# Performance work log

Hardware: AMD Instinct MI355X
Metric: run time of the kernel (lower is better)

## Reference

```python
import jax, jax.numpy as jnp
import numpy as np

NUM_POINTS = 7
SCALES = (0.25, 0.125, 0.0625, 0.03125)
LENS_AREA = (8, 25)
OUTPUT_SIZES = ((8, 32), (8, 64))
CANON_SCALE = 224.0  # LevelMapper defaults (ctor's 160 is not forwarded)
CANON_LVL = 4.0
K_MIN, K_MAX = 2.0, 5.0
EPS = 1e-6


def _boundary_interp(pts, wp):
    # pts: [N, n, 2] polyline; sample wp points uniformly in arc parameter
    n = pts.shape[1]
    u = (jnp.arange(wp, dtype=pts.dtype) + 0.5) / wp * (n - 1)
    i0 = jnp.clip(jnp.floor(u).astype(jnp.int32), 0, n - 2)
    f = (u - i0.astype(pts.dtype))[None, :, None]
    return pts[:, i0] * (1 - f) + pts[:, i0 + 1] * f  # [N, wp, 2]


def _make_grid(polys_norm, hp, wp):
    # polys_norm: [N, 2n, 2] normalized to [0,1]; first n = top l->r, last n = bottom l->r
    n = polys_norm.shape[1] // 2
    top = _boundary_interp(polys_norm[:, :n], wp)
    bot = _boundary_interp(polys_norm[:, n:], wp)
    v = ((jnp.arange(hp, dtype=polys_norm.dtype) + 0.5) / hp)[None, :, None, None]
    return top[:, None] * (1 - v) + bot[:, None] * v  # [N, hp, wp, 2] (x,y)


def _bilinear(feat, img_ids, grid):
    # feat [B,C,H,W]; grid normalized [0,1] image coords -> pixel coords of this level
    B, C, H, W = feat.shape
    x = grid[..., 0] * W - 0.5
    y = grid[..., 1] * H - 0.5
    x0 = jnp.floor(x)
    y0 = jnp.floor(y)
    wx = (x - x0)[..., None]
    wy = (y - y0)[..., None]
    x0i = x0.astype(jnp.int32)
    y0i = y0.astype(jnp.int32)
    ids = img_ids[:, None, None]

    def g(xi, yi):
        xc = jnp.clip(xi, 0, W - 1)
        yc = jnp.clip(yi, 0, H - 1)
        val = feat[ids, :, yc, xc]  # [N, hp, wp, C]
        m = ((xi >= 0) & (xi < W) & (yi >= 0) & (yi < H))[..., None]
        return val * m.astype(feat.dtype)

    out = (g(x0i, y0i) * (1 - wx) * (1 - wy)
           + g(x0i + 1, y0i) * wx * (1 - wy)
           + g(x0i, y0i + 1) * (1 - wx) * wy
           + g(x0i + 1, y0i + 1) * wx * wy)
    return jnp.transpose(out, (0, 3, 1, 2))  # [N, C, hp, wp]


def _forward(feats, polys, img_ids, lens):
    n = NUM_POINTS
    idx = list(range(n)) + list(range(n, 2 * n))[::-1]  # top l->r, bottom flipped l->r
    H0, W0 = feats[0].shape[-2:]
    wh = jnp.array([W0 / SCALES[0], H0 / SCALES[0]], dtype=feats[0].dtype)
    polys_norm = polys[:, idx] / wh
    # FPN level routing from bbox area of the polygon (boxlist.area heuristic)
    s = jnp.sqrt((polys[..., 0].max(1) - polys[..., 0].min(1))
                 * (polys[..., 1].max(1) - polys[..., 1].min(1)))
    lvl = jnp.clip(jnp.floor(CANON_LVL + jnp.log2(s / CANON_SCALE + EPS)),
                   K_MIN, K_MAX).astype(jnp.int32) - int(K_MIN)
    # text-length bucket -> pooler id (first bucket whose len_max >= len)
    thr = jnp.array(LENS_AREA[:-1], dtype=lens.dtype)
    pooler_id = jnp.sum(lens[:, None] > thr[None, :], axis=1).astype(jnp.int32)

    outs = []
    N, C = polys.shape[0], feats[0].shape[1]
    for pid, (hp, wp) in enumerate(OUTPUT_SIZES):
        grid = _make_grid(polys_norm, hp, wp)
        acc = jnp.zeros((N, C, hp, wp), feats[0].dtype)
        for l, f in enumerate(feats):
            sel = ((lvl == l) & (pooler_id == pid))[:, None, None, None]
            acc = jnp.where(sel, _bilinear(f, img_ids, grid), acc)
        outs.append(acc)
    return tuple(outs)


def setup_inputs() -> dict:
    B, C, H0, W0 = 2, 256, 200, 336
    N, n = 256, NUM_POINTS
    key = jax.random.key(0)
    k0, k1, k2, k3 = jax.random.split(key, 4)
    feat0 = jax.random.normal(k0, (B, C, H0, W0), jnp.float32)
    feat1 = jax.random.normal(k1, (B, C, H0 // 2, W0 // 2), jnp.float32)
    feat2 = jax.random.normal(k2, (B, C, H0 // 4, W0 // 4), jnp.float32)
    feat3 = jax.random.normal(k3, (B, C, H0 // 8, W0 // 8), jnp.float32)
    rng = np.random.default_rng(0)
    img_w, img_h = W0 / SCALES[0], H0 / SCALES[0]
    cx = rng.uniform(0.25, 0.75, N) * img_w
    cy = rng.uniform(0.2, 0.8, N) * img_h
    w = rng.uniform(40.0, 600.0, N)
    h = rng.uniform(16.0, 80.0, N)
    t = np.linspace(0.0, 1.0, n)
    top_x = cx[:, None] + (t[None, :] - 0.5) * w[:, None]
    top_y = cy[:, None] - h[:, None] / 2 + rng.uniform(-2, 2, (N, n))
    bot_y = cy[:, None] + h[:, None] / 2 + rng.uniform(-2, 2, (N, n))
    # stored polygon order: top l->r then bottom r->l (matches self.idx reorder)
    top = np.stack([top_x, top_y], -1)
    bot = np.stack([top_x[:, ::-1], bot_y[:, ::-1]], -1)
    polys = jnp.asarray(np.concatenate([top, bot], 1), jnp.float32)  # [N, 14, 2]
    img_ids = jnp.asarray(rng.integers(0, B, N), jnp.int32)
    lens = jnp.asarray(rng.integers(1, 25, N), jnp.int32)
    return {"feat0": feat0, "feat1": feat1, "feat2": feat2, "feat3": feat3,
            "polys": polys, "img_ids": img_ids, "lens": lens}


def reference(feat0, feat1, feat2, feat3, polys, img_ids, lens):
    return _forward((feat0, feat1, feat2, feat3), polys, img_ids, lens)
```

## Files before the change

kernel.cpp:

```cpp
#include <hip/hip_runtime.h>


#define NBOX 256
#define NCH  256
#define HP   8
#define CCHUNK 32
#define OUT0_ELEMS ((size_t)NBOX * NCH * HP * 32)

__global__ __launch_bounds__(256) void poly_pool_kernel(
    const float* __restrict__ f0, const float* __restrict__ f1,
    const float* __restrict__ f2, const float* __restrict__ f3,
    const float* __restrict__ polys, const int* __restrict__ img_ids,
    const int* __restrict__ lens, float* __restrict__ out)
{
    const int b    = blockIdx.y;
    const int pidk = blockIdx.z;
    const int wp   = pidk ? 64 : 32;
    const int npos = HP * wp;
    const int c0   = blockIdx.x * CCHUNK;
    const int tid  = threadIdx.x;

    float* outb = out + (pidk ? OUT0_ELEMS : 0) + (size_t)b * NCH * npos;

    const int pooler = (lens[b] > 8) ? 1 : 0;
    if (pooler != pidk) {
        float* p = outb + (size_t)c0 * npos;
        const int total = CCHUNK * npos;
        for (int k = tid; k < total; k += 256) p[k] = 0.0f;
        return;
    }

    __shared__ float pts[28];
    __shared__ int   soff[512][4];
    __shared__ float swt [512][4];

    if (tid < 28) pts[tid] = polys[b * 28 + tid];
    __syncthreads();

    float minx = pts[0], maxx = pts[0], miny = pts[1], maxy = pts[1];
#pragma unroll
    for (int k = 1; k < 14; ++k) {
        float x = pts[2 * k], y = pts[2 * k + 1];
        minx = fminf(minx, x); maxx = fmaxf(maxx, x);
        miny = fminf(miny, y); maxy = fmaxf(maxy, y);
    }
    float s = sqrtf((maxx - minx) * (maxy - miny));
    int lvl = (int)floorf(4.0f + log2f(s / 224.0f + 1e-6f));
    lvl = min(max(lvl, 2), 5) - 2;

    const float* feat; int H, W;
    switch (lvl) {
        case 0:  feat = f0; H = 200; W = 336; break;
        case 1:  feat = f1; H = 100; W = 168; break;
        case 2:  feat = f2; H = 50;  W = 84;  break;
        default: feat = f3; H = 25;  W = 42;  break;
    }
    const int img = img_ids[b];
    const float* featimg = feat + (size_t)img * NCH * H * W;

    const float Wf = (float)W, Hf = (float)H;
    for (int pos = tid; pos < npos; pos += 256) {
        int i = pos / wp, j = pos % wp;

        float u = ((j + 0.5f) / (float)wp) * 6.0f;
        int   i0 = (int)floorf(u);
        i0 = min(max(i0, 0), 5);
        float f = u - (float)i0;

        float txa = pts[2 * i0]       / 1344.0f, tya = pts[2 * i0 + 1] / 800.0f;
        float txb = pts[2 * i0 + 2]   / 1344.0f, tyb = pts[2 * i0 + 3] / 800.0f;
        int ka = 13 - i0, kb = 12 - i0;
        float bxa = pts[2 * ka] / 1344.0f, bya = pts[2 * ka + 1] / 800.0f;
        float bxb = pts[2 * kb] / 1344.0f, byb = pts[2 * kb + 1] / 800.0f;

        float topx = txa * (1.0f - f) + txb * f;
        float topy = tya * (1.0f - f) + tyb * f;
        float botx = bxa * (1.0f - f) + bxb * f;
        float boty = bya * (1.0f - f) + byb * f;

        float v  = (i + 0.5f) / 8.0f;
        float gx = topx * (1.0f - v) + botx * v;
        float gy = topy * (1.0f - v) + boty * v;

        float x = gx * Wf - 0.5f;
        float y = gy * Hf - 0.5f;
        float x0f = floorf(x), y0f = floorf(y);
        float fx = x - x0f,   fy = y - y0f;
        int x0 = (int)x0f, y0 = (int)y0f;
        int x1 = x0 + 1,   y1 = y0 + 1;

        int x0c = min(max(x0, 0), W - 1), x1c = min(max(x1, 0), W - 1);
        int y0c = min(max(y0, 0), H - 1), y1c = min(max(y1, 0), H - 1);
        float m00 = (x0 >= 0 && x0 < W && y0 >= 0 && y0 < H) ? 1.0f : 0.0f;
        float m10 = (x1 >= 0 && x1 < W && y0 >= 0 && y0 < H) ? 1.0f : 0.0f;
        float m01 = (x0 >= 0 && x0 < W && y1 >= 0 && y1 < H) ? 1.0f : 0.0f;
        float m11 = (x1 >= 0 && x1 < W && y1 >= 0 && y1 < H) ? 1.0f : 0.0f;

        soff[pos][0] = y0c * W + x0c;
        soff[pos][1] = y0c * W + x1c;
        soff[pos][2] = y1c * W + x0c;
        soff[pos][3] = y1c * W + x1c;
        swt [pos][0] = (1.0f - fx) * (1.0f - fy) * m00;
        swt [pos][1] = fx * (1.0f - fy) * m10;
        swt [pos][2] = (1.0f - fx) * fy * m01;
        swt [pos][3] = fx * fy * m11;
    }
    __syncthreads();

    const int p0 = tid;
    int   o00 = soff[p0][0], o10 = soff[p0][1], o01 = soff[p0][2], o11 = soff[p0][3];
    float w00 = swt[p0][0],  w10 = swt[p0][1],  w01 = swt[p0][2],  w11 = swt[p0][3];
    const bool two = (npos == 512);
    int   q00 = 0, q10 = 0, q01 = 0, q11 = 0;
    float v00 = 0, v10 = 0, v01 = 0, v11 = 0;
    if (two) {
        const int p1 = tid + 256;
        q00 = soff[p1][0]; q10 = soff[p1][1]; q01 = soff[p1][2]; q11 = soff[p1][3];
        v00 = swt[p1][0];  v10 = swt[p1][1];  v01 = swt[p1][2];  v11 = swt[p1][3];
    }

    for (int c = c0; c < c0 + CCHUNK; ++c) {
        const float* fc = featimg + (size_t)c * H * W;
        float r0 = w00 * fc[o00] + w10 * fc[o10] + w01 * fc[o01] + w11 * fc[o11];
        outb[(size_t)c * npos + p0] = r0;
        if (two) {
            float r1 = v00 * fc[q00] + v10 * fc[q10] + v01 * fc[q01] + v11 * fc[q11];
            outb[(size_t)c * npos + p0 + 256] = r1;
        }
    }
}

extern "C" void kernel_launch(void* const* d_in, const int* in_sizes, int n_in,
                              void* d_out, int out_size, void* d_ws, size_t ws_size,
                              hipStream_t stream) {
    const float* f0    = (const float*)d_in[0];
    const float* f1    = (const float*)d_in[1];
    const float* f2    = (const float*)d_in[2];
    const float* f3    = (const float*)d_in[3];
    const float* polys = (const float*)d_in[4];
    const int*   ids   = (const int*)d_in[5];
    const int*   lens  = (const int*)d_in[6];
    float* out = (float*)d_out;

    dim3 grid(NCH / CCHUNK, NBOX, 2);
    poly_pool_kernel<<<grid, 256, 0, stream>>>(f0, f1, f2, f3, polys, ids, lens, out);
}
```

Measured before the change: 365.9 us.

## Compute sampling geometry in registers, batch gathers, use nontemporal vector stores

Drops the shared-memory offset and weight tables: each thread now computes the bilinear geometry for its own positions directly in registers, which removes the second barrier. The channel loop is unrolled so 8 (or 4×2) channels of gathers are issued before any FMA, giving more loads in flight to hide latency. Zero-fill of inactive pooler outputs uses 16-byte vector nontemporal stores, and the output writes are nontemporal too. The unrolled temporaries raise register pressure.

```diff
diff --git a/kernel.cpp b/kernel.cpp
--- a/kernel.cpp
+++ b/kernel.cpp
@@ -7,6 +7,59 @@
 #define CCHUNK 32
 #define OUT0_ELEMS ((size_t)NBOX * NCH * HP * 32)
 
+typedef float f32x4 __attribute__((ext_vector_type(4)));
+
+__device__ __forceinline__ void make_geo(
+    const float* __restrict__ pts, int pos, int lwp, int W, int H,
+    int& o00, int& o10, int& o01, int& o11,
+    float& w00, float& w10, float& w01, float& w11)
+{
+    const int wp = 1 << lwp;
+    const int i  = pos >> lwp;
+    const int j  = pos & (wp - 1);
+
+    float u  = ((j + 0.5f) / (float)wp) * 6.0f;
+    int   i0 = (int)floorf(u);
+    i0 = min(max(i0, 0), 5);
+    float f = u - (float)i0;
+
+    float txa = pts[2 * i0]     / 1344.0f, tya = pts[2 * i0 + 1] / 800.0f;
+    float txb = pts[2 * i0 + 2] / 1344.0f, tyb = pts[2 * i0 + 3] / 800.0f;
+    int ka = 13 - i0, kb = 12 - i0;
+    float bxa = pts[2 * ka] / 1344.0f, bya = pts[2 * ka + 1] / 800.0f;
+    float bxb = pts[2 * kb] / 1344.0f, byb = pts[2 * kb + 1] / 800.0f;
+
+    float topx = txa * (1.0f - f) + txb * f;
+    float topy = tya * (1.0f - f) + tyb * f;
+    float botx = bxa * (1.0f - f) + bxb * f;
+    float boty = bya * (1.0f - f) + byb * f;
+
+    float v  = (i + 0.5f) / 8.0f;
+    float gx = topx * (1.0f - v) + botx * v;
+    float gy = topy * (1.0f - v) + boty * v;
+
+    float x = gx * (float)W - 0.5f;
+    float y = gy * (float)H - 0.5f;
+    float x0f = floorf(x), y0f = floorf(y);
+    float fx = x - x0f,   fy = y - y0f;
+    int x0 = (int)x0f, y0 = (int)y0f;
+    int x1 = x0 + 1,   y1 = y0 + 1;
+
+    int x0c = min(max(x0, 0), W - 1), x1c = min(max(x1, 0), W - 1);
+    int y0c = min(max(y0, 0), H - 1), y1c = min(max(y1, 0), H - 1);
+    float m00 = (x0 >= 0 && x0 < W && y0 >= 0 && y0 < H) ? 1.0f : 0.0f;
+    float m10 = (x1 >= 0 && x1 < W && y0 >= 0 && y0 < H) ? 1.0f : 0.0f;
+    float m01 = (x0 >= 0 && x0 < W && y1 >= 0 && y1 < H) ? 1.0f : 0.0f;
+    float m11 = (x1 >= 0 && x1 < W && y1 >= 0 && y1 < H) ? 1.0f : 0.0f;
+
+    o00 = y0c * W + x0c;  o10 = y0c * W + x1c;
+    o01 = y1c * W + x0c;  o11 = y1c * W + x1c;
+    w00 = (1.0f - fx) * (1.0f - fy) * m00;
+    w10 = fx * (1.0f - fy) * m10;
+    w01 = (1.0f - fx) * fy * m01;
+    w11 = fx * fy * m11;
+}
+
 __global__ __launch_bounds__(256) void poly_pool_kernel(
     const float* __restrict__ f0, const float* __restrict__ f1,
     const float* __restrict__ f2, const float* __restrict__ f3,
@@ -15,25 +68,24 @@
 {
     const int b    = blockIdx.y;
     const int pidk = blockIdx.z;
-    const int wp   = pidk ? 64 : 32;
-    const int npos = HP * wp;
+    const int lwp  = 5 + pidk;
+    const int npos = HP << lwp;
     const int c0   = blockIdx.x * CCHUNK;
     const int tid  = threadIdx.x;
 
-    float* outb = out + (pidk ? OUT0_ELEMS : 0) + (size_t)b * NCH * npos;
+    float* outb = out + (pidk ? OUT0_ELEMS : (size_t)0) + (size_t)b * NCH * npos;
 
     const int pooler = (lens[b] > 8) ? 1 : 0;
     if (pooler != pidk) {
-        float* p = outb + (size_t)c0 * npos;
-        const int total = CCHUNK * npos;
-        for (int k = tid; k < total; k += 256) p[k] = 0.0f;
+        f32x4 z = (f32x4)(0.0f);
+        f32x4* p = reinterpret_cast<f32x4*>(outb + (size_t)c0 * npos);
+        const int total4 = (CCHUNK * npos) >> 2;
+        for (int k = tid; k < total4; k += 256)
+            __builtin_nontemporal_store(z, p + k);
         return;
     }
 
     __shared__ float pts[28];
-    __shared__ int   soff[512][4];
-    __shared__ float swt [512][4];
-
     if (tid < 28) pts[tid] = polys[b * 28 + tid];
     __syncthreads();
 
@@ -56,76 +108,54 @@
         default: feat = f3; H = 25;  W = 42;  break;
     }
     const int img = img_ids[b];
-    const float* featimg = feat + (size_t)img * NCH * H * W;
+    const int HW  = H * W;
+    const float* featimg = feat + (size_t)img * NCH * HW;
+    const float* fbase   = featimg + (size_t)c0 * HW;
 
-    const float Wf = (float)W, Hf = (float)H;
-    for (int pos = tid; pos < npos; pos += 256) {
-        int i = pos / wp, j = pos % wp;
+    int   o00, o10, o01, o11;
+    float w00, w10, w01, w11;
+    make_geo(pts, tid, lwp, W, H, o00, o10, o01, o11, w00, w10, w01, w11);
 
-        float u = ((j + 0.5f) / (float)wp) * 6.0f;
-        int   i0 = (int)floorf(u);
-        i0 = min(max(i0, 0), 5);
-        float f = u - (float)i0;
+    float* op = outb + (size_t)c0 * npos + tid;
 
-        float txa = pts[2 * i0]       / 1344.0f, tya = pts[2 * i0 + 1] / 800.0f;
-        float txb = pts[2 * i0 + 2]   / 1344.0f, tyb = pts[2 * i0 + 3] / 800.0f;
-        int ka = 13 - i0, kb = 12 - i0;
-        float bxa = pts[2 * ka] / 1344.0f, bya = pts[2 * ka + 1] / 800.0f;
-        float bxb = pts[2 * kb] / 1344.0f, byb = pts[2 * kb + 1] / 800.0f;
+    if (!pidk) {
+        for (int c = 0; c < CCHUNK; c += 8) {
+            float t00[8], t10[8], t01[8], t11[8];
+#pragma unroll
+            for (int k = 0; k < 8; ++k) {
+                const float* fc = fbase + (size_t)(c + k) * HW;
+                t00[k] = fc[o00]; t10[k] = fc[o10];
+                t01[k] = fc[o01]; t11[k] = fc[o11];
+            }
+#pragma unroll
+            for (int k = 0; k < 8; ++k) {
+                float r = w00 * t00[k] + w10 * t10[k] + w01 * t01[k] + w11 * t11[k];
+                __builtin_nontemporal_store(r, op + (size_t)(c + k) * 256);
+            }
+        }
+    } else {
+        int   q00, q10, q01, q11;
+        float v00, v10, v01, v11;
+        make_geo(pts, tid + 256, lwp, W, H, q00, q10, q01, q11, v00, v10, v01, v11);
 
-        float topx = txa * (1.0f - f) + txb * f;
-        float topy = tya * (1.0f - f) + tyb * f;
-        float botx = bxa * (1.0f - f) + bxb * f;
-        float boty = bya * (1.0f - f) + byb * f;
-
-        float v  = (i + 0.5f) / 8.0f;
-        float gx = topx * (1.0f - v) + botx * v;
-        float gy = topy * (1.0f - v) + boty * v;
-
-        float x = gx * Wf - 0.5f;
-        float y = gy * Hf - 0.5f;
-        float x0f = floorf(x), y0f = floorf(y);
-        float fx = x - x0f,   fy = y - y0f;
-        int x0 = (int)x0f, y0 = (int)y0f;
-        int x1 = x0 + 1,   y1 = y0 + 1;
-
-        int x0c = min(max(x0, 0), W - 1), x1c = min(max(x1, 0), W - 1);
-        int y0c = min(max(y0, 0), H - 1), y1c = min(max(y1, 0), H - 1);
-        float m00 = (x0 >= 0 && x0 < W && y0 >= 0 && y0 < H) ? 1.0f : 0.0f;
-        float m10 = (x1 >= 0 && x1 < W && y0 >= 0 && y0 < H) ? 1.0f : 0.0f;
-        float m01 = (x0 >= 0 && x0 < W && y1 >= 0 && y1 < H) ? 1.0f : 0.0f;
-        float m11 = (x1 >= 0 && x1 < W && y1 >= 0 && y1 < H) ? 1.0f : 0.0f;
-
-        soff[pos][0] = y0c * W + x0c;
-        soff[pos][1] = y0c * W + x1c;
-        soff[pos][2] = y1c * W + x0c;
-        soff[pos][3] = y1c * W + x1c;
-        swt [pos][0] = (1.0f - fx) * (1.0f - fy) * m00;
-        swt [pos][1] = fx * (1.0f - fy) * m10;
-        swt [pos][2] = (1.0f - fx) * fy * m01;
-        swt [pos][3] = fx * fy * m11;
-    }
-    __syncthreads();
-
-    const int p0 = tid;
-    int   o00 = soff[p0][0], o10 = soff[p0][1], o01 = soff[p0][2], o11 = soff[p0][3];
-    float w00 = swt[p0][0],  w10 = swt[p0][1],  w01 = swt[p0][2],  w11 = swt[p0][3];
-    const bool two = (npos == 512);
-    int   q00 = 0, q10 = 0, q01 = 0, q11 = 0;
-    float v00 = 0, v10 = 0, v01 = 0, v11 = 0;
-    if (two) {
-        const int p1 = tid + 256;
-        q00 = soff[p1][0]; q10 = soff[p1][1]; q01 = soff[p1][2]; q11 = soff[p1][3];
-        v00 = swt[p1][0];  v10 = swt[p1][1];  v01 = swt[p1][2];  v11 = swt[p1][3];
-    }
-
-    for (int c = c0; c < c0 + CCHUNK; ++c) {
-        const float* fc = featimg + (size_t)c * H * W;
-        float r0 = w00 * fc[o00] + w10 * fc[o10] + w01 * fc[o01] + w11 * fc[o11];
-        outb[(size_t)c * npos + p0] = r0;
-        if (two) {
-            float r1 = v00 * fc[q00] + v10 * fc[q10] + v01 * fc[q01] + v11 * fc[q11];
-            outb[(size_t)c * npos + p0 + 256] = r1;
+        for (int c = 0; c < CCHUNK; c += 4) {
+            float t00[4], t10[4], t01[4], t11[4];
+            float s00[4], s10[4], s01[4], s11[4];
+#pragma unroll
+            for (int k = 0; k < 4; ++k) {
+                const float* fc = fbase + (size_t)(c + k) * HW;
+                t00[k] = fc[o00]; t10[k] = fc[o10];
+                t01[k] = fc[o01]; t11[k] = fc[o11];
+                s00[k] = fc[q00]; s10[k] = fc[q10];
+                s01[k] = fc[q01]; s11[k] = fc[q11];
+            }
+#pragma unroll
+            for (int k = 0; k < 4; ++k) {
+                float r0 = w00 * t00[k] + w10 * t10[k] + w01 * t01[k] + w11 * t11[k];
+                float r1 = v00 * s00[k] + v10 * s10[k] + v01 * s01[k] + v11 * s11[k];
+                __builtin_nontemporal_store(r0, op + (size_t)(c + k) * 512);
+                __builtin_nontemporal_store(r1, op + (size_t)(c + k) * 512 + 256);
+            }
         }
     }
 }
```

New measurement: 355.0 us. -3.0%, faster.
